# Kernel optimization log

Measured on AMD Instinct MI355X. Metric: run time of the kernel, lower is better.

## Reference

```python
import math
import jax, jax.numpy as jnp
import numpy as np

B, T, E = 2, 2048, 2048
NUM_HEADS = 16
H = NUM_HEADS // 2          # differential head pairs = 8
D = E // NUM_HEADS          # head_dim = 128
DEPTH = 12
LAMBDA_INIT = 0.8 - 0.6 * math.exp(-0.3 * DEPTH)
EPS = 1e-5


def setup_inputs() -> dict:
    key = jax.random.key(0)
    ks = jax.random.split(key, 10)
    sc = lambda k, shape, std: jax.random.normal(k, shape, dtype=jnp.float32) * std
    return {
        "x": jax.random.normal(ks[0], (B, T, E), dtype=jnp.float32),
        "Wq": sc(ks[1], (E, E), 0.02),   # [in, out]
        "Wk": sc(ks[2], (E, E), 0.02),   # n_rep == 1 -> k/v proj width = embed_dim
        "Wv": sc(ks[3], (E, E), 0.02),
        "Wo": sc(ks[4], (E, E), 0.02),
        "lambda_q1": sc(ks[5], (D,), 0.1),
        "lambda_k1": sc(ks[6], (D,), 0.1),
        "lambda_q2": sc(ks[7], (D,), 0.1),
        "lambda_k2": sc(ks[8], (D,), 0.1),
        "g": jnp.ones((2 * D,), dtype=jnp.float32),  # RMSNorm weight
    }


def _forward(x, Wq, Wk, Wv, Wo, lq1, lk1, lq2, lk2, g):
    Bz, Tl, _ = x.shape
    # projections; view(bsz, T, 2*H, D).reshape(bsz, T, H, 2, D): adjacent head
    # pairs become the two differential components.
    q = (x @ Wq).reshape(Bz, Tl, H, 2, D)
    k = (x @ Wk).reshape(Bz, Tl, H, 2, D)
    v = (x @ Wv).reshape(Bz, Tl, H, 2 * D)   # value width is 2*head_dim

    scale = D ** -0.5                         # SDPA default scaling
    causal = jnp.tril(jnp.ones((Tl, Tl), dtype=bool))  # is_causal=True

    def attend(qc, kc):
        # qc, kc: [B, T, H, D]
        s = jnp.einsum('bthd,bshd->bhts', qc, kc) * scale
        s = jnp.where(causal, s, -jnp.inf)
        a = jax.nn.softmax(s, axis=-1)
        return jnp.einsum('bhts,bshe->bthe', a, v)  # [B, T, H, 2D]

    # interleaved q/k + repeated v in the single SDPA == two attention maps on full V
    o1 = attend(q[..., 0, :], k[..., 0, :])
    o2 = attend(q[..., 1, :], k[..., 1, :])

    lam = jnp.exp(jnp.sum(lq1 * lk1)) - jnp.exp(jnp.sum(lq2 * lk2)) + LAMBDA_INIT
    o = o1 - lam * o2
    # RMSNorm over last dim (2*head_dim), eps=1e-5, learned weight g
    o = o * jax.lax.rsqrt(jnp.mean(o * o, axis=-1, keepdims=True) + EPS) * g
    o = o * (1.0 - LAMBDA_INIT)
    return o.reshape(Bz, Tl, E) @ Wo


def reference(x, Wq, Wk, Wv, Wo, lambda_q1, lambda_k1, lambda_q2, lambda_k2, g):
    return _forward(x, Wq, Wk, Wv, Wo, lambda_q1, lambda_k1, lambda_q2, lambda_k2, g)
```

## Files before the change

### kernel.cpp

```cpp
#include <hip/hip_runtime.h>
#include <stdint.h>
#include <math.h>


typedef unsigned short u16;
typedef short bf16x8 __attribute__((ext_vector_type(8)));
typedef float f32x4 __attribute__((ext_vector_type(4)));

typedef uint32_t __attribute__((address_space(1))) as1_u32;
typedef uint32_t __attribute__((address_space(3))) as3_u32;

#define LAMBDA_INIT 0.78360576653162453f

__device__ __forceinline__ u16 f2bf(float f) {
  uint32_t u = __float_as_uint(f);
  u += 0x7FFFu + ((u >> 16) & 1u);
  return (u16)(u >> 16);
}
__device__ __forceinline__ float bf2f(u16 v) {
  return __uint_as_float(((uint32_t)v) << 16);
}

__device__ __forceinline__ void async16(u16* lds, const u16* g) {
  __builtin_amdgcn_global_load_lds((const as1_u32*)(uintptr_t)g,
                                   (as3_u32*)(uint32_t)(uintptr_t)lds, 16, 0, 0);
}

__device__ __forceinline__ f32x4 mfma16(bf16x8 a, bf16x8 b, f32x4 c) {
  return __builtin_amdgcn_mfma_f32_16x16x32_bf16(a, b, c, 0, 0, 0);
}


__global__ void cast_x_kernel(const float* __restrict__ x, u16* __restrict__ xb, int n4) {
  int i = blockIdx.x * 256 + threadIdx.x;
  if (i < n4) {
    float4 v = ((const float4*)x)[i];
    ushort4 o;
    o.x = f2bf(v.x); o.y = f2bf(v.y); o.z = f2bf(v.z); o.w = f2bf(v.w);
    ((ushort4*)xb)[i] = o;
  }
}

__global__ void transpose_w_kernel(const float* __restrict__ W, u16* __restrict__ Wt) {
  __shared__ float tile[32][33];
  int tx = threadIdx.x, ty = threadIdx.y;
  int c0 = blockIdx.x * 32, r0 = blockIdx.y * 32;
#pragma unroll
  for (int i = 0; i < 32; i += 8)
    tile[ty + i][tx] = W[(size_t)(r0 + ty + i) * 2048 + c0 + tx];
  __syncthreads();
#pragma unroll
  for (int i = 0; i < 32; i += 8)
    Wt[(size_t)(c0 + ty + i) * 2048 + r0 + tx] = f2bf(tile[tx][ty + i]);
}

__global__ void lam_kernel(const float* __restrict__ lq1, const float* __restrict__ lk1,
                           const float* __restrict__ lq2, const float* __restrict__ lk2,
                           float* __restrict__ out) {
  int L = threadIdx.x;
  float d1 = lq1[L] * lk1[L] + lq1[L + 64] * lk1[L + 64];
  float d2 = lq2[L] * lk2[L] + lq2[L + 64] * lk2[L + 64];
#pragma unroll
  for (int m = 1; m < 64; m <<= 1) {
    d1 += __shfl_xor(d1, m);
    d2 += __shfl_xor(d2, m);
  }
  if (L == 0) out[0] = __expf(d1) - __expf(d2) + LAMBDA_INIT;
}

template <int OUT_BF16>
__global__ __launch_bounds__(256, 2) void gemm_bt_kernel(const u16* __restrict__ A,
                                                         const u16* __restrict__ Bt,
                                                         void* __restrict__ Cout,
                                                         int M, int N, int K) {
  __shared__ __attribute__((aligned(16))) u16 As[128 * 32];
  __shared__ __attribute__((aligned(16))) u16 Bs[128 * 32];
  int t = threadIdx.x;
  int lane = t & 63, w = t >> 6;
  int lr = lane & 15, lq = lane >> 4;
  int m0 = blockIdx.y * 128, n0 = blockIdx.x * 128;
  int wm = (w >> 1) * 64, wn = (w & 1) * 64;
  const u16* Ab = A + (size_t)m0 * K;
  const u16* Bb = Bt + (size_t)n0 * K;
  f32x4 acc[4][4] = {};
  int r0 = t >> 2;
  int kc0 = (t & 3) * 8;

  for (int k0 = 0; k0 < K; k0 += 32) {
    __syncthreads();
    async16(&As[t * 8], Ab + (size_t)r0 * K + k0 + kc0);
    async16(&Bs[t * 8], Bb + (size_t)r0 * K + k0 + kc0);
    async16(&As[(256 + t) * 8], Ab + (size_t)(64 + r0) * K + k0 + kc0);
    async16(&Bs[(256 + t) * 8], Bb + (size_t)(64 + r0) * K + k0 + kc0);
    __syncthreads();
    bf16x8 a[4], b[4];
#pragma unroll
    for (int mi = 0; mi < 4; mi++)
      a[mi] = *(const bf16x8*)&As[(wm + mi * 16 + lr) * 32 + lq * 8];
#pragma unroll
    for (int ni = 0; ni < 4; ni++)
      b[ni] = *(const bf16x8*)&Bs[(wn + ni * 16 + lr) * 32 + lq * 8];
#pragma unroll
    for (int mi = 0; mi < 4; mi++)
#pragma unroll
      for (int ni = 0; ni < 4; ni++)
        acc[mi][ni] = mfma16(a[mi], b[ni], acc[mi][ni]);
  }
#pragma unroll
  for (int mi = 0; mi < 4; mi++) {
#pragma unroll
    for (int ni = 0; ni < 4; ni++) {
#pragma unroll
      for (int r = 0; r < 4; r++) {
        int row = m0 + wm + mi * 16 + lq * 4 + r;
        int col = n0 + wn + ni * 16 + lr;
        if (OUT_BF16)
          ((u16*)Cout)[(size_t)row * N + col] = f2bf(acc[mi][ni][r]);
        else
          ((float*)Cout)[(size_t)row * N + col] = acc[mi][ni][r];
      }
    }
  }
}


struct FlashCtx {
  const u16* Qbase;
  const u16* Kbase;
  const u16* Vbase;
  int t, w, lr, lq;
};

__device__ __forceinline__ void stage_kv(const FlashCtx& cx, int jc,
                                         u16* KsN, u16* VsN) {
#pragma unroll
  for (int i = 0; i < 2; i++) {
    int q = cx.t + i * 256;
    int row = q >> 4, gp = q & 15;
    int gg = (gp & 8) | ((gp & 7) ^ (row & 7));
    async16(&KsN[q * 8], cx.Kbase + (size_t)(jc + row) * 4096 + gg * 8);
  }
#pragma unroll
  for (int i = 0; i < 4; i++) {
    int q = cx.t + i * 256;
    int e = q >> 2, gp = q & 3;
    int gg = gp ^ ((e >> 1) & 3);
    async16(&VsN[q * 8], cx.Vbase + (size_t)e * 4096 + jc + gg * 8);
  }
}

__device__ __forceinline__ void flash_step(const FlashCtx& cx, const bf16x8* qa,
                                           int jc, int njc, int q0,
                                           const u16* KsC, const u16* VsC,
                                           u16* KsN, u16* VsN, u16* PsW,
                                           f32x4* acc, f32x4* lacc, float* m_) {
  __syncthreads();
  if (njc >= 0) stage_kv(cx, njc, KsN, VsN);

  if (jc > q0 + cx.w * 16 + 15) return;
  const float k2 = 0.12753257550036097f;
  int lr = cx.lr, lq = cx.lq;

  f32x4 sacc[2] = {};
#pragma unroll
  for (int ks = 0; ks < 4; ks++) {
#pragma unroll
    for (int ni = 0; ni < 2; ni++) {
      int row = ni * 16 + lr;
      int g = ks * 4 + lq;
      int gp = (g & 8) | ((g & 7) ^ (row & 7));
      bf16x8 kb = *(const bf16x8*)&KsC[row * 128 + gp * 8];
      sacc[ni] = mfma16(qa[ks], kb, sacc[ni]);
    }
  }

  float s2[2][4];
  bool diag = (jc >= q0);
#pragma unroll
  for (int ni = 0; ni < 2; ni++)
#pragma unroll
    for (int r = 0; r < 4; r++) {
      float v = sacc[ni][r] * k2;
      if (diag) {
        int colg = jc + ni * 16 + lr;
        int rowg = q0 + cx.w * 16 + lq * 4 + r;
        if (colg > rowg) v = -INFINITY;
      }
      s2[ni][r] = v;
    }

  float mv = fmaxf(fmaxf(fmaxf(s2[0][0], s2[0][1]), fmaxf(s2[0][2], s2[0][3])),
                   fmaxf(fmaxf(s2[1][0], s2[1][1]), fmaxf(s2[1][2], s2[1][3])));
  mv = fmaxf(mv, __shfl_xor(mv, 1));
  mv = fmaxf(mv, __shfl_xor(mv, 2));
  mv = fmaxf(mv, __shfl_xor(mv, 4));
  mv = fmaxf(mv, __shfl_xor(mv, 8));
  mv = fmaxf(mv, __shfl_xor(mv, 16));
  mv = fmaxf(mv, __shfl_xor(mv, 32));
  float mo = *m_;
  float mn = fmaxf(mo, mv);
  *m_ = mn;
  float a = __builtin_amdgcn_exp2f(mo - mn);

#pragma unroll
  for (int ni = 0; ni < 2; ni++)
#pragma unroll
    for (int r = 0; r < 4; r++) {
      float p = __builtin_amdgcn_exp2f(s2[ni][r] - mn);
      PsW[(lq * 4 + r) * 40 + ni * 16 + lr] = (u16)(__float_as_uint(p) >> 16);
    }

  if (a != 1.0f) {
#pragma unroll
    for (int ei = 0; ei < 16; ei++)
#pragma unroll
      for (int r = 0; r < 4; r++) acc[ei][r] *= a;
#pragma unroll
    for (int r = 0; r < 4; r++) (*lacc)[r] *= a;
  }

  const bf16x8 onesb = {0x3F80, 0x3F80, 0x3F80, 0x3F80, 0x3F80, 0x3F80, 0x3F80, 0x3F80};
  bf16x8 pa = *(const bf16x8*)&PsW[lr * 40 + lq * 8];
#pragma unroll
  for (int ei = 0; ei < 16; ei++) {
    int row = ei * 16 + lr;
    int gp = lq ^ ((row >> 1) & 3);
    bf16x8 vb = *(const bf16x8*)&VsC[row * 32 + gp * 8];
    acc[ei] = mfma16(pa, vb, acc[ei]);
  }
  *lacc = mfma16(pa, onesb, *lacc);
}

__global__ __launch_bounds__(256, 2) void flash_diff_kernel(const u16* __restrict__ QKb,
                                                            const u16* __restrict__ Vt,
                                                            u16* __restrict__ o12b) {
  __shared__ __attribute__((aligned(16))) u16 Ks0[32 * 128];
  __shared__ __attribute__((aligned(16))) u16 Ks1[32 * 128];
  __shared__ __attribute__((aligned(16))) u16 Vs0[256 * 32];
  __shared__ __attribute__((aligned(16))) u16 Vs1[256 * 32];
  __shared__ __attribute__((aligned(16))) u16 Ps[4][16 * 40];

  int t = threadIdx.x;
  FlashCtx cx;
  cx.t = t; cx.w = t >> 6;
  cx.lr = t & 15; cx.lq = (t >> 4) & 3;

  int idx = blockIdx.x;
  int xcd = idx & 7, slot = idx >> 3;
  int pairI = slot & 15, ghi = slot >> 4;
  int g = ghi * 8 + xcd;
  int bh = g >> 1, c = g & 1;
  int b = bh >> 3, h = bh & 7;

  cx.Qbase = QKb + (size_t)b * 2048 * 4096 + h * 256 + c * 128;
  cx.Kbase = cx.Qbase + 2048;
  cx.Vbase = Vt + (size_t)(h * 256) * 4096 + b * 2048;
  u16* Op = o12b + (size_t)c * (4096ull * 2048) + (size_t)b * 2048 * 2048 + h * 256;
  u16* PsW = Ps[cx.w];

  stage_kv(cx, 0, Ks0, Vs0);

#pragma unroll 1
  for (int phase = 0; phase < 2; phase++) {
    int qi = phase ? (31 - pairI) : pairI;
    int q0 = qi * 64;
    int nst = 2 * qi + 2;

    bf16x8 qa[4];
#pragma unroll
    for (int ks = 0; ks < 4; ks++)
      qa[ks] = *(const bf16x8*)&cx.Qbase[(size_t)(q0 + cx.w * 16 + cx.lr) * 4096 +
                                         ks * 32 + cx.lq * 8];

    f32x4 acc[16] = {};
    f32x4 lacc = {};
    float m_ = -INFINITY;

#pragma unroll 1
    for (int jj = 0; jj < nst; jj += 2) {
      int n0c = (jj + 1 < nst) ? (jj + 1) * 32 : -1;
      int n1c;
      if (jj + 2 < nst) n1c = (jj + 2) * 32;
      else n1c = (phase == 0) ? 0 : -1;
      flash_step(cx, qa, jj * 32, n0c, q0, Ks0, Vs0, Ks1, Vs1, PsW, acc, &lacc, &m_);
      flash_step(cx, qa, (jj + 1) * 32, n1c, q0, Ks1, Vs1, Ks0, Vs0, PsW, acc, &lacc, &m_);
    }

#pragma unroll
    for (int r = 0; r < 4; r++) {
      float inv = 1.0f / lacc[r];
      int row = q0 + cx.w * 16 + cx.lq * 4 + r;
#pragma unroll
      for (int ei = 0; ei < 16; ei++)
        Op[(size_t)row * 2048 + ei * 16 + cx.lr] = f2bf(acc[ei][r] * inv);
    }
  }
}

__global__ void combine_kernel(const u16* __restrict__ o12b, const float* __restrict__ lamp,
                               const float* __restrict__ g, u16* __restrict__ ob) {
  __shared__ float red[4];
  int t = threadIdx.x;
  int grp = blockIdx.x;
  size_t idx = (size_t)grp * 256 + t;
  const size_t comp = 4096ull * 2048;
  float lam = lamp[0];
  float v = bf2f(o12b[idx]) - lam * bf2f(o12b[idx + comp]);
  float ss = v * v;
  ss += __shfl_xor(ss, 1);
  ss += __shfl_xor(ss, 2);
  ss += __shfl_xor(ss, 4);
  ss += __shfl_xor(ss, 8);
  ss += __shfl_xor(ss, 16);
  ss += __shfl_xor(ss, 32);
  if ((t & 63) == 0) red[t >> 6] = ss;
  __syncthreads();
  float tot = red[0] + red[1] + red[2] + red[3];
  float scale = rsqrtf(tot * (1.0f / 256.0f) + 1e-5f) * (1.0f - LAMBDA_INIT);
  ob[(size_t)(grp >> 3) * 2048 + (grp & 7) * 256 + t] = f2bf(v * scale * g[t]);
}


extern "C" void kernel_launch(void* const* d_in, const int* in_sizes, int n_in,
                              void* d_out, int out_size, void* d_ws, size_t ws_size,
                              hipStream_t stream) {
  const float* x   = (const float*)d_in[0];
  const float* Wq  = (const float*)d_in[1];
  const float* Wk  = (const float*)d_in[2];
  const float* Wv  = (const float*)d_in[3];
  const float* Wo  = (const float*)d_in[4];
  const float* lq1 = (const float*)d_in[5];
  const float* lk1 = (const float*)d_in[6];
  const float* lq2 = (const float*)d_in[7];
  const float* lk2 = (const float*)d_in[8];
  const float* g   = (const float*)d_in[9];

  char* ws = (char*)d_ws;
  u16* xb    = (u16*)(ws);
  u16* Wtq   = (u16*)(ws + 16777216);
  u16* Wtk   = (u16*)(ws + 25165824);
  u16* Wtv   = (u16*)(ws + 33554432);
  u16* Wto   = (u16*)(ws + 41943040);
  u16* QKb   = (u16*)(ws + 50331648);
  u16* Vt    = (u16*)(ws + 83886080);
  u16* o12b  = (u16*)(ws + 100663296);
  u16* ob    = (u16*)(ws + 134217728);
  float* lamp = (float*)(ws + 150994944);

  cast_x_kernel<<<8192, 256, 0, stream>>>(x, xb, 2097152);
  dim3 tb(32, 8), tg(64, 64);
  transpose_w_kernel<<<tg, tb, 0, stream>>>(Wq, Wtq);
  transpose_w_kernel<<<tg, tb, 0, stream>>>(Wk, Wtk);
  transpose_w_kernel<<<tg, tb, 0, stream>>>(Wv, Wtv);
  transpose_w_kernel<<<tg, tb, 0, stream>>>(Wo, Wto);
  lam_kernel<<<1, 64, 0, stream>>>(lq1, lk1, lq2, lk2, lamp);

  gemm_bt_kernel<1><<<dim3(32, 32), 256, 0, stream>>>(xb, Wtq, QKb, 4096, 4096, 2048);
  gemm_bt_kernel<1><<<dim3(32, 16), 256, 0, stream>>>(Wtv, xb, Vt, 2048, 4096, 2048);

  flash_diff_kernel<<<512, 256, 0, stream>>>(QKb, Vt, o12b);
  combine_kernel<<<32768, 256, 0, stream>>>(o12b, lamp, g, ob);
  gemm_bt_kernel<0><<<dim3(16, 32), 256, 0, stream>>>(ob, Wto, (float*)d_out, 4096, 2048, 2048);
}
```

Measured before the change: 451.6 us.

## Use 64-wide KV tiles, overlap V load with QK, lazy rescale

The flash kernel moves from 32-key to 64-key tiles. K stays double-buffered across iterations, while V is single-buffered and loaded during the current QK^T and softmax, with a second barrier before the PV MFMAs. The online-softmax max update and accumulator rescale are skipped unless some score exceeds the running max by more than 8 (exp2 domain). This halves loop iterations and barriers per tile and removes most rescale work, at the cost of more LDS, V load latency exposed within each step, and a threshold-based max that relies on bounded growth in the unnormalised sums.

```diff
diff --git a/kernel.cpp b/kernel.cpp
--- a/kernel.cpp
+++ b/kernel.cpp
@@ -131,114 +131,33 @@
   int t, w, lr, lq;
 };
 
-__device__ __forceinline__ void stage_kv(const FlashCtx& cx, int jc,
-                                         u16* KsN, u16* VsN) {
-#pragma unroll
-  for (int i = 0; i < 2; i++) {
+__device__ __forceinline__ void stage_k(const FlashCtx& cx, int jc, u16* Kn) {
+#pragma unroll
+  for (int i = 0; i < 4; i++) {
     int q = cx.t + i * 256;
     int row = q >> 4, gp = q & 15;
     int gg = (gp & 8) | ((gp & 7) ^ (row & 7));
-    async16(&KsN[q * 8], cx.Kbase + (size_t)(jc + row) * 4096 + gg * 8);
-  }
-#pragma unroll
-  for (int i = 0; i < 4; i++) {
+    async16(&Kn[q * 8], cx.Kbase + (size_t)(jc + row) * 4096 + gg * 8);
+  }
+}
+
+__device__ __forceinline__ void stage_v(const FlashCtx& cx, int jc, u16* Vs) {
+#pragma unroll
+  for (int i = 0; i < 8; i++) {
     int q = cx.t + i * 256;
-    int e = q >> 2, gp = q & 3;
-    int gg = gp ^ ((e >> 1) & 3);
-    async16(&VsN[q * 8], cx.Vbase + (size_t)e * 4096 + jc + gg * 8);
-  }
-}
-
-__device__ __forceinline__ void flash_step(const FlashCtx& cx, const bf16x8* qa,
-                                           int jc, int njc, int q0,
-                                           const u16* KsC, const u16* VsC,
-                                           u16* KsN, u16* VsN, u16* PsW,
-                                           f32x4* acc, f32x4* lacc, float* m_) {
-  __syncthreads();
-  if (njc >= 0) stage_kv(cx, njc, KsN, VsN);
-
-  if (jc > q0 + cx.w * 16 + 15) return;
-  const float k2 = 0.12753257550036097f;
-  int lr = cx.lr, lq = cx.lq;
-
-  f32x4 sacc[2] = {};
-#pragma unroll
-  for (int ks = 0; ks < 4; ks++) {
-#pragma unroll
-    for (int ni = 0; ni < 2; ni++) {
-      int row = ni * 16 + lr;
-      int g = ks * 4 + lq;
-      int gp = (g & 8) | ((g & 7) ^ (row & 7));
-      bf16x8 kb = *(const bf16x8*)&KsC[row * 128 + gp * 8];
-      sacc[ni] = mfma16(qa[ks], kb, sacc[ni]);
-    }
-  }
-
-  float s2[2][4];
-  bool diag = (jc >= q0);
-#pragma unroll
-  for (int ni = 0; ni < 2; ni++)
-#pragma unroll
-    for (int r = 0; r < 4; r++) {
-      float v = sacc[ni][r] * k2;
-      if (diag) {
-        int colg = jc + ni * 16 + lr;
-        int rowg = q0 + cx.w * 16 + lq * 4 + r;
-        if (colg > rowg) v = -INFINITY;
-      }
-      s2[ni][r] = v;
-    }
-
-  float mv = fmaxf(fmaxf(fmaxf(s2[0][0], s2[0][1]), fmaxf(s2[0][2], s2[0][3])),
-                   fmaxf(fmaxf(s2[1][0], s2[1][1]), fmaxf(s2[1][2], s2[1][3])));
-  mv = fmaxf(mv, __shfl_xor(mv, 1));
-  mv = fmaxf(mv, __shfl_xor(mv, 2));
-  mv = fmaxf(mv, __shfl_xor(mv, 4));
-  mv = fmaxf(mv, __shfl_xor(mv, 8));
-  mv = fmaxf(mv, __shfl_xor(mv, 16));
-  mv = fmaxf(mv, __shfl_xor(mv, 32));
-  float mo = *m_;
-  float mn = fmaxf(mo, mv);
-  *m_ = mn;
-  float a = __builtin_amdgcn_exp2f(mo - mn);
-
-#pragma unroll
-  for (int ni = 0; ni < 2; ni++)
-#pragma unroll
-    for (int r = 0; r < 4; r++) {
-      float p = __builtin_amdgcn_exp2f(s2[ni][r] - mn);
-      PsW[(lq * 4 + r) * 40 + ni * 16 + lr] = (u16)(__float_as_uint(p) >> 16);
-    }
-
-  if (a != 1.0f) {
-#pragma unroll
-    for (int ei = 0; ei < 16; ei++)
-#pragma unroll
-      for (int r = 0; r < 4; r++) acc[ei][r] *= a;
-#pragma unroll
-    for (int r = 0; r < 4; r++) (*lacc)[r] *= a;
-  }
-
-  const bf16x8 onesb = {0x3F80, 0x3F80, 0x3F80, 0x3F80, 0x3F80, 0x3F80, 0x3F80, 0x3F80};
-  bf16x8 pa = *(const bf16x8*)&PsW[lr * 40 + lq * 8];
-#pragma unroll
-  for (int ei = 0; ei < 16; ei++) {
-    int row = ei * 16 + lr;
-    int gp = lq ^ ((row >> 1) & 3);
-    bf16x8 vb = *(const bf16x8*)&VsC[row * 32 + gp * 8];
-    acc[ei] = mfma16(pa, vb, acc[ei]);
-  }
-  *lacc = mfma16(pa, onesb, *lacc);
+    int e = q >> 3, gp = q & 7;
+    int gg = gp ^ (e & 7);
+    async16(&Vs[q * 8], cx.Vbase + (size_t)e * 4096 + jc + gg * 8);
+  }
 }
 
 __global__ __launch_bounds__(256, 2) void flash_diff_kernel(const u16* __restrict__ QKb,
                                                             const u16* __restrict__ Vt,
                                                             u16* __restrict__ o12b) {
-  __shared__ __attribute__((aligned(16))) u16 Ks0[32 * 128];
-  __shared__ __attribute__((aligned(16))) u16 Ks1[32 * 128];
-  __shared__ __attribute__((aligned(16))) u16 Vs0[256 * 32];
-  __shared__ __attribute__((aligned(16))) u16 Vs1[256 * 32];
-  __shared__ __attribute__((aligned(16))) u16 Ps[4][16 * 40];
+  __shared__ __attribute__((aligned(16))) u16 Ks0[64 * 128];
+  __shared__ __attribute__((aligned(16))) u16 Ks1[64 * 128];
+  __shared__ __attribute__((aligned(16))) u16 Vs[256 * 64];
+  __shared__ __attribute__((aligned(16))) u16 Ps[4][16 * 88];
 
   int t = threadIdx.x;
   FlashCtx cx;
@@ -258,13 +177,16 @@
   u16* Op = o12b + (size_t)c * (4096ull * 2048) + (size_t)b * 2048 * 2048 + h * 256;
   u16* PsW = Ps[cx.w];
 
-  stage_kv(cx, 0, Ks0, Vs0);
+  u16* Kc = Ks0;
+  u16* Kn = Ks1;
+
+  stage_k(cx, 0, Kc);
 
 #pragma unroll 1
   for (int phase = 0; phase < 2; phase++) {
     int qi = phase ? (31 - pairI) : pairI;
     int q0 = qi * 64;
-    int nst = 2 * qi + 2;
+    int nst = qi + 1;
 
     bf16x8 qa[4];
 #pragma unroll
@@ -275,15 +197,105 @@
     f32x4 acc[16] = {};
     f32x4 lacc = {};
     float m_ = -INFINITY;
+    int rowmax = q0 + cx.w * 16 + 15;
 
 #pragma unroll 1
-    for (int jj = 0; jj < nst; jj += 2) {
-      int n0c = (jj + 1 < nst) ? (jj + 1) * 32 : -1;
-      int n1c;
-      if (jj + 2 < nst) n1c = (jj + 2) * 32;
-      else n1c = (phase == 0) ? 0 : -1;
-      flash_step(cx, qa, jj * 32, n0c, q0, Ks0, Vs0, Ks1, Vs1, PsW, acc, &lacc, &m_);
-      flash_step(cx, qa, (jj + 1) * 32, n1c, q0, Ks1, Vs1, Ks0, Vs0, PsW, acc, &lacc, &m_);
+    for (int j = 0; j < nst; j++) {
+      int jc = j * 64;
+      int njc = (j + 1 < nst) ? (j + 1) * 64 : (phase == 0 ? 0 : -1);
+
+      __syncthreads();
+      if (njc >= 0) stage_k(cx, njc, Kn);
+      stage_v(cx, jc, Vs);
+
+      bool act = (jc <= rowmax);
+      if (act) {
+        f32x4 sacc[4] = {};
+#pragma unroll
+        for (int ks = 0; ks < 4; ks++) {
+#pragma unroll
+          for (int ni = 0; ni < 4; ni++) {
+            int row = ni * 16 + cx.lr;
+            int gk = ks * 4 + cx.lq;
+            int gp = (gk & 8) | ((gk & 7) ^ (row & 7));
+            bf16x8 kb = *(const bf16x8*)&Kc[row * 128 + gp * 8];
+            sacc[ni] = mfma16(qa[ks], kb, sacc[ni]);
+          }
+        }
+
+        const float k2 = 0.12753257550036097f;
+        float s2[4][4];
+        bool diag = (jc + 63 > q0 + cx.w * 16);
+#pragma unroll
+        for (int ni = 0; ni < 4; ni++)
+#pragma unroll
+          for (int r = 0; r < 4; r++) {
+            float v = sacc[ni][r] * k2;
+            if (diag) {
+              int colg = jc + ni * 16 + cx.lr;
+              int rowg = q0 + cx.w * 16 + cx.lq * 4 + r;
+              if (colg > rowg) v = -INFINITY;
+            }
+            s2[ni][r] = v;
+          }
+
+        float sm = fmaxf(
+            fmaxf(fmaxf(fmaxf(s2[0][0], s2[0][1]), fmaxf(s2[0][2], s2[0][3])),
+                  fmaxf(fmaxf(s2[1][0], s2[1][1]), fmaxf(s2[1][2], s2[1][3]))),
+            fmaxf(fmaxf(fmaxf(s2[2][0], s2[2][1]), fmaxf(s2[2][2], s2[2][3])),
+                  fmaxf(fmaxf(s2[3][0], s2[3][1]), fmaxf(s2[3][2], s2[3][3]))));
+        float mo = m_;
+        if (__any(sm > mo + 8.0f)) {
+          float mv = sm;
+          mv = fmaxf(mv, __shfl_xor(mv, 1));
+          mv = fmaxf(mv, __shfl_xor(mv, 2));
+          mv = fmaxf(mv, __shfl_xor(mv, 4));
+          mv = fmaxf(mv, __shfl_xor(mv, 8));
+          mv = fmaxf(mv, __shfl_xor(mv, 16));
+          mv = fmaxf(mv, __shfl_xor(mv, 32));
+          float mn = fmaxf(mo, mv);
+          float a = __builtin_amdgcn_exp2f(mo - mn);
+#pragma unroll
+          for (int ei = 0; ei < 16; ei++)
+#pragma unroll
+            for (int r = 0; r < 4; r++) acc[ei][r] *= a;
+#pragma unroll
+          for (int r = 0; r < 4; r++) lacc[r] *= a;
+          m_ = mn;
+          mo = mn;
+        }
+
+#pragma unroll
+        for (int ni = 0; ni < 4; ni++)
+#pragma unroll
+          for (int r = 0; r < 4; r++) {
+            float p = __builtin_amdgcn_exp2f(s2[ni][r] - mo);
+            PsW[(cx.lq * 4 + r) * 88 + ni * 16 + cx.lr] =
+                (u16)(__float_as_uint(p) >> 16);
+          }
+      }
+
+      __syncthreads();
+      if (act) {
+        const bf16x8 onesb = {0x3F80, 0x3F80, 0x3F80, 0x3F80,
+                              0x3F80, 0x3F80, 0x3F80, 0x3F80};
+        bf16x8 pa0 = *(const bf16x8*)&PsW[cx.lr * 88 + cx.lq * 8];
+        bf16x8 pa1 = *(const bf16x8*)&PsW[cx.lr * 88 + 32 + cx.lq * 8];
+#pragma unroll
+        for (int ei = 0; ei < 16; ei++) {
+          int e = ei * 16 + cx.lr;
+          int g0 = cx.lq ^ (e & 7);
+          int g1 = g0 ^ 4;
+          bf16x8 vb0 = *(const bf16x8*)&Vs[e * 64 + g0 * 8];
+          bf16x8 vb1 = *(const bf16x8*)&Vs[e * 64 + g1 * 8];
+          acc[ei] = mfma16(pa0, vb0, acc[ei]);
+          acc[ei] = mfma16(pa1, vb1, acc[ei]);
+        }
+        lacc = mfma16(pa0, onesb, lacc);
+        lacc = mfma16(pa1, onesb, lacc);
+      }
+
+      u16* tmp = Kc; Kc = Kn; Kn = tmp;
     }
 
 #pragma unroll
```

After: 433.0 us. 1.04x faster.
